# Performance work log

Measured on AMD Instinct MI355X. Metric: run time of the kernel, lower is better.

## Reference

```python
import jax, jax.numpy as jnp
import numpy as np

L = 16            # num_levels
F = 2             # features per level
T = 1 << 19       # hashmap size
BASE = 16         # base resolution
RES = 512         # desired_resolution (outer trilinear grid)
N_PTS = 262144

# 8 corner offsets of a unit cube, [8,3]
OFFS = np.array([[(c >> 0) & 1, (c >> 1) & 1, (c >> 2) & 1] for c in range(8)], dtype=np.uint32)
OFFS_J = jnp.asarray(OFFS)
OFFS_B = jnp.asarray(OFFS.astype(bool))
P1 = jnp.uint32(2654435761)
P2 = jnp.uint32(805459861)


def hash_encode(x01, table):
    """Instant-NGP multiresolution hash encoding. x01: [N,3] in [0,1]. table: [L,T,F]."""
    feats = []
    for l in range(L):
        res = BASE * (2 ** l)
        pos = x01 * res                      # [N,3]
        p0 = jnp.floor(pos)
        frac = pos - p0                      # [N,3]
        corners = p0.astype(jnp.uint32)[:, None, :] + OFFS_J[None]   # [N,8,3]
        if (res + 1) ** 3 <= T:              # dense level
            c = jnp.minimum(corners, jnp.uint32(res))
            idx = c[..., 0] + c[..., 1] * jnp.uint32(res + 1) + c[..., 2] * jnp.uint32((res + 1) * (res + 1))
        else:                                # hashed level (spatial hash, xor of primes)
            idx = corners[..., 0] ^ (corners[..., 1] * P1) ^ (corners[..., 2] * P2)
            idx = idx & jnp.uint32(T - 1)
        g = table[l][idx.astype(jnp.int32)]  # [N,8,F]
        w = jnp.where(OFFS_B[None], frac[:, None, :], 1.0 - frac[:, None, :]).prod(-1)  # [N,8]
        feats.append(jnp.einsum('nc,ncf->nf', w, g))
    return jnp.concatenate(feats, axis=-1)   # [N, L*F]


def mlp(x, W0, W1, W2):
    h = jax.nn.relu(x @ W0)
    h = jax.nn.relu(h @ W1)
    return h @ W2


def setup_inputs() -> dict:
    key = jax.random.key(0)
    k1, k2, k3, k4, k5 = jax.random.split(key, 5)
    xyz = jax.random.uniform(k1, (N_PTS, 3), dtype=jnp.float32, minval=-1.0, maxval=1.0)
    table = jax.random.uniform(k2, (L, T, F), dtype=jnp.float32, minval=-1e-4, maxval=1e-4)
    W0 = jax.random.normal(k3, (L * F, 64), dtype=jnp.float32) * (1.0 / np.sqrt(L * F))
    W1 = jax.random.normal(k4, (64, 64), dtype=jnp.float32) * (1.0 / 8.0)
    W2 = jax.random.normal(k5, (64, 8), dtype=jnp.float32) * (1.0 / 8.0)
    return {"xyz": xyz, "table": table, "W0": W0, "W1": W1, "W2": W2, "bound": 1}


def reference(xyz, table, W0, W1, W2, bound):
    xn = (xyz + bound) / (2 * bound)          # [N,3] in [0,1]
    coords = xn * RES
    c0 = jnp.clip(jnp.floor(coords), 0.0, RES - 1.0)   # [N,3] floats holding ints
    frac = coords - c0                         # u,v,w per-axis [N,3]
    out = jnp.zeros((xyz.shape[0], 8), dtype=xyz.dtype)
    for b in range(8):
        bits = np.array([(b >> 0) & 1, (b >> 1) & 1, (b >> 2) & 1], dtype=np.float32)
        cc = (c0 + bits) / RES                 # corner point normalized to [0,1]
        f = mlp(hash_encode(cc, table), W0, W1, W2)   # [N,8]
        w = jnp.where(bits.astype(bool), frac, 1.0 - frac).prod(-1)  # [N]
        out = out + w[:, None] * f
    return out
```

## Files before the change

### kernel.cpp

```cpp
#include <hip/hip_runtime.h>


typedef __attribute__((ext_vector_type(8))) short short8_t;
typedef __attribute__((ext_vector_type(4))) float f32x4;
typedef unsigned long long ull;

static constexpr unsigned kT    = 1u << 19;
static constexpr unsigned kMask = kT - 1u;
static constexpr unsigned cP1   = 2654435761u;
static constexpr unsigned cP2   = 805459861u;
static constexpr int      BLOCK = 256;
static constexpr int      TOFF  = 4096;
static constexpr unsigned CMB   = 1u << 20;
static constexpr unsigned SMF   = 1u << 21;
static constexpr unsigned D01   = (1u << 21) + (1u << 17);
static constexpr unsigned N01   = 35937u;
static constexpr unsigned D2    = D01 + 72000u;
static constexpr unsigned N2    = 274625u;
static constexpr unsigned PARTO = 2621440u;
static constexpr size_t   WS_NEED2 = ((size_t)PARTO + (1u << 22)) * 4;

static __device__ __forceinline__ unsigned bf16_rn(float x) {
    unsigned u = __float_as_uint(x);
    return (u + 0x7fffu + ((u >> 16) & 1u)) >> 16;
}

static __device__ __forceinline__ float2 bf2dec(unsigned u) {
    return make_float2(__uint_as_float(u << 16),
                       __uint_as_float(u & 0xffff0000u));
}

static __device__ __forceinline__ unsigned cvtpk(float lo, float hi) {
    unsigned r;
    asm("v_cvt_pk_bf16_f32 %0, %1, %2" : "=v"(r) : "v"(lo), "v"(hi));
    return r;
}

static __device__ __forceinline__ unsigned pkbf(ull e) {
    return bf16_rn(__uint_as_float((unsigned)e))
         | (bf16_rn(__uint_as_float((unsigned)(e >> 32))) << 16);
}

static __device__ __forceinline__ f32x4 mfma16(short8_t a, short8_t b, f32x4 c) {
    return __builtin_amdgcn_mfma_f32_16x16x32_bf16(a, b, c, 0, 0, 0);
}

__global__ __launch_bounds__(256)
void prep_all(const float* __restrict__ W0, const float* __restrict__ W1,
              const float* __restrict__ W2, const float2* __restrict__ tbl,
              unsigned* __restrict__ ws, int ncc, int ncb, int nsf, int ncd,
              int nc01)
{
    const int bx = blockIdx.x, tid = threadIdx.x;
    if (bx < ncc) {
        const int i = bx * 256 + tid;
        const ull* __restrict__ p = (const ull*)(tbl + (size_t)3 * kT);
        const ull a = __builtin_nontemporal_load(p + 2 * (size_t)i);
        const ull b = __builtin_nontemporal_load(p + 2 * (size_t)i + 1);
        ((ull*)(ws + TOFF))[i] = (ull)pkbf(a) | ((ull)pkbf(b) << 32);
    } else if (bx < ncc + ncb) {
        const unsigned j = (unsigned)((bx - ncc) * 256 + tid);
        unsigned dw[8];
        #pragma unroll
        for (int b = 0; b < 4; ++b) {
            const ull e = __builtin_nontemporal_load(
                (const ull*)tbl + (size_t)5 * kT + (j | ((unsigned)b << 17)));
            dw[b] = pkbf(e);
        }
        #pragma unroll
        for (int b = 0; b < 2; ++b) {
            const ull e = __builtin_nontemporal_load(
                (const ull*)tbl + (size_t)6 * kT
                + ((size_t)(j | ((unsigned)b << 17)) << 1));
            dw[4 + b] = pkbf(e);
        }
        {
            const ull e = __builtin_nontemporal_load(
                (const ull*)tbl + (size_t)7 * kT + ((size_t)j << 2));
            dw[6] = pkbf(e);
            dw[7] = 0u;
        }
        uint4* dst = (uint4*)(ws + TOFF + CMB + j * 8);
        dst[0] = make_uint4(dw[0], dw[1], dw[2], dw[3]);
        dst[1] = make_uint4(dw[4], dw[5], dw[6], dw[7]);
    } else if (bx < ncc + ncb + nsf) {
        const int i = (bx - ncc - ncb) * 256 + tid;
        const unsigned v = 131071u - (unsigned)i;
        const int s = __clz((int)v) - 12;
        const unsigned fo = (1u << 17) - (1u << (20 - s));
        const unsigned j = (unsigned)i - fo;
        const ull e = __builtin_nontemporal_load(
            (const ull*)tbl + ((size_t)(5 + s) << 19) + ((size_t)j << s));
        ws[TOFF + SMF + i] = pkbf(e);
    } else if (bx < ncc + ncb + nsf + ncd) {
        const int i = (bx - ncc - ncb - nsf) * 256 + tid;
        if (i < (int)N2) {
            const ull e = __builtin_nontemporal_load(
                (const ull*)tbl + (size_t)2 * kT + i);
            ws[TOFF + D2 + i] = pkbf(e);
        }
    } else if (bx < ncc + ncb + nsf + ncd + nc01) {
        const int i = (bx - ncc - ncb - nsf - ncd) * 256 + tid;
        if (i < (int)N01) {
            const int vz = i / 1089;
            const int r  = i - vz * 1089;
            const int vy = r / 33;
            const int vx = r - vy * 33;
            const float2 f1 = tbl[(size_t)kT + i];
            const int x0 = vx >> 1, y0 = vy >> 1, z0 = vz >> 1;
            const int x1 = (x0 + 1 > 16) ? 16 : x0 + 1;
            const int y1 = (y0 + 1 > 16) ? 16 : y0 + 1;
            const int z1 = (z0 + 1 > 16) ? 16 : z0 + 1;
            const float fx = (vx & 1) ? 0.5f : 0.0f;
            const float fy = (vy & 1) ? 0.5f : 0.0f;
            const float fz = (vz & 1) ? 0.5f : 0.0f;
            const int Y0 = y0 * 17, Y1 = y1 * 17, Z0 = z0 * 289, Z1 = z1 * 289;
            const float2 g0 = tbl[x0 + Y0 + Z0], g1 = tbl[x1 + Y0 + Z0];
            const float2 g2 = tbl[x0 + Y1 + Z0], g3 = tbl[x1 + Y1 + Z0];
            const float2 g4 = tbl[x0 + Y0 + Z1], g5 = tbl[x1 + Y0 + Z1];
            const float2 g6 = tbl[x0 + Y1 + Z1], g7 = tbl[x1 + Y1 + Z1];
            const float wx1 = fx, wx0 = 1.0f - fx;
            const float wy1 = fy, wy0 = 1.0f - fy;
            const float wz1 = fz, wz0 = 1.0f - fz;
            const float w00 = wx0 * wy0, w10 = wx1 * wy0, w01 = wx0 * wy1, w11 = wx1 * wy1;
            const float a0 = w00 * wz0, a1 = w10 * wz0, a2 = w01 * wz0, a3 = w11 * wz0;
            const float a4 = w00 * wz1, a5 = w10 * wz1, a6 = w01 * wz1, a7 = w11 * wz1;
            const float f0x = a0 * g0.x + a1 * g1.x + a2 * g2.x + a3 * g3.x
                            + a4 * g4.x + a5 * g5.x + a6 * g6.x + a7 * g7.x;
            const float f0y = a0 * g0.y + a1 * g1.y + a2 * g2.y + a3 * g3.y
                            + a4 * g4.y + a5 * g5.y + a6 * g6.y + a7 * g7.y;
            ((ull*)(ws + TOFF + D01))[i] =
                (ull)cvtpk(f0x, f0y) | ((ull)cvtpk(f1.x, f1.y) << 32);
        }
    } else {
        const int t = (bx - ncc - ncb - nsf - ncd - nc01) * 4 + (tid >> 6);
        if (t >= 14) return;
        const int lane = tid & 63;
        const int n = lane & 15, q = lane >> 4;
        unsigned hi[4];
        #pragma unroll
        for (int d = 0; d < 4; ++d) {
            unsigned h2[2];
            #pragma unroll
            for (int s = 0; s < 2; ++s) {
                const int j = d * 2 + s;
                float v;
                if (t < 4) {
                    v = W0[(q * 8 + j) * 64 + t * 16 + n];
                } else {
                    const int kp = (j < 4) ? (q * 4 + j) : (16 + q * 4 + (j - 4));
                    if (t < 12) v = W1[(((t - 4) & 1) * 32 + kp) * 64 + ((t - 4) >> 1) * 16 + n];
                    else        v = (n < 8) ? W2[((t - 12) * 32 + kp) * 8 + n] : 0.0f;
                }
                h2[s] = bf16_rn(v);
            }
            hi[d] = h2[0] | (h2[1] << 16);
        }
        ((uint4*)ws)[t * 64 + lane] = make_uint4(hi[0], hi[1], hi[2], hi[3]);
    }
}

__global__ __launch_bounds__(256, 8)
void ngp_pa(const float* __restrict__ xyz, const int* __restrict__ boundp,
            unsigned* __restrict__ ws)
{
    const int tid = threadIdx.x;
    const int ge  = blockIdx.x * 256 + tid;
    const int pt  = ge >> 3;
    const int b   = ge & 7;

    const float bnd = (float)boundp[0];
    const float sc  = 0.5f / bnd;
    const float pxv = __builtin_nontemporal_load(xyz + pt * 3 + 0);
    const float pyv = __builtin_nontemporal_load(xyz + pt * 3 + 1);
    const float pzv = __builtin_nontemporal_load(xyz + pt * 3 + 2);
    const float cxf = (pxv + bnd) * sc * 512.0f;
    const float cyf = (pyv + bnd) * sc * 512.0f;
    const float czf = (pzv + bnd) * sc * 512.0f;
    const float c0x = fminf(fmaxf(floorf(cxf), 0.0f), 511.0f);
    const float c0y = fminf(fmaxf(floorf(cyf), 0.0f), 511.0f);
    const float c0z = fminf(fmaxf(floorf(czf), 0.0f), 511.0f);
    const unsigned kx = (unsigned)c0x + (unsigned)(b & 1);
    const unsigned ky = (unsigned)c0y + (unsigned)((b >> 1) & 1);
    const unsigned kz = (unsigned)c0z + (unsigned)((b >> 2) & 1);

    const unsigned* __restrict__ tbx = ws + TOFF;
    unsigned gH[2][8];
    #pragma unroll
    for (int l = 3; l < 5; ++l) {
        const int d = 5 - l;
        const unsigned qx = kx >> d, qy = ky >> d, qz = kz >> d;
        const unsigned hy0 = qy * cP1, hy1 = hy0 + cP1;
        const unsigned hz0 = qz * cP2, hz1 = hz0 + cP2;
        const unsigned x1u = qx + 1u;
        unsigned hidx[8];
        hidx[0] = (qx  ^ hy0 ^ hz0) & kMask;  hidx[1] = (x1u ^ hy0 ^ hz0) & kMask;
        hidx[2] = (qx  ^ hy1 ^ hz0) & kMask;  hidx[3] = (x1u ^ hy1 ^ hz0) & kMask;
        hidx[4] = (qx  ^ hy0 ^ hz1) & kMask;  hidx[5] = (x1u ^ hy0 ^ hz1) & kMask;
        hidx[6] = (qx  ^ hy1 ^ hz1) & kMask;  hidx[7] = (x1u ^ hy1 ^ hz1) & kMask;
        const unsigned* __restrict__ base = tbx + (size_t)(l - 3) * kT;
        #pragma unroll
        for (int c = 0; c < 8; ++c) gH[l - 3][c] = base[hidx[c]];
    }

    unsigned xd34[2];
    #pragma unroll
    for (int l = 3; l < 5; ++l) {
        const int d = 5 - l;
        const unsigned m = (1u << d) - 1u;
        const float inv = 1.0f / (float)(1 << d);
        const float fx = (float)(kx & m) * inv;
        const float fy = (float)(ky & m) * inv;
        const float fz = (float)(kz & m) * inv;
        const float2 g0 = bf2dec(gH[l - 3][0]), g1 = bf2dec(gH[l - 3][1]);
        const float2 g2 = bf2dec(gH[l - 3][2]), g3 = bf2dec(gH[l - 3][3]);
        const float2 g4 = bf2dec(gH[l - 3][4]), g5 = bf2dec(gH[l - 3][5]);
        const float2 g6 = bf2dec(gH[l - 3][6]), g7 = bf2dec(gH[l - 3][7]);
        const float wx1 = fx, wx0 = 1.0f - fx;
        const float wy1 = fy, wy0 = 1.0f - fy;
        const float wz1 = fz, wz0 = 1.0f - fz;
        const float w00 = wx0 * wy0, w10 = wx1 * wy0, w01 = wx0 * wy1, w11 = wx1 * wy1;
        const float a0 = w00 * wz0, a1 = w10 * wz0, a2 = w01 * wz0, a3 = w11 * wz0;
        const float a4 = w00 * wz1, a5 = w10 * wz1, a6 = w01 * wz1, a7 = w11 * wz1;
        const float vx = a0 * g0.x + a1 * g1.x + a2 * g2.x + a3 * g3.x
                       + a4 * g4.x + a5 * g5.x + a6 * g6.x + a7 * g7.x;
        const float vy = a0 * g0.y + a1 * g1.y + a2 * g2.y + a3 * g3.y
                       + a4 * g4.y + a5 * g5.y + a6 * g6.y + a7 * g7.y;
        xd34[l - 3] = cvtpk(vx, vy);
    }
    ((ull*)(ws + PARTO))[ge] = (ull)xd34[0] | ((ull)xd34[1] << 32);
}

__global__ __launch_bounds__(BLOCK, 5)
void ngp_pb(const float*  __restrict__ xyz,
            const int*    __restrict__ boundp,
            const unsigned* __restrict__ wsw,
            float*        __restrict__ out)
{
    __shared__ __align__(16) unsigned lds[4096];
    const int tid  = threadIdx.x;
    const int lane = tid & 63;
    const int wv   = tid >> 6;
    const int col  = lane & 15;
    const int q    = lane >> 4;
    const int swz  = (tid ^ (tid >> 2) ^ (tid >> 4)) & 3;

    const unsigned* __restrict__ tbx = wsw + TOFF;
    const float bnd = (float)boundp[0];
    const float sc  = 0.5f / bnd;
    const f32x4 zero = {0.0f, 0.0f, 0.0f, 0.0f};

    const int ge = blockIdx.x * BLOCK + tid;
    const int pt = ge >> 3;
    const int b  = ge & 7;

    const float pxv = __builtin_nontemporal_load(xyz + pt * 3 + 0);
    const float pyv = __builtin_nontemporal_load(xyz + pt * 3 + 1);
    const float pzv = __builtin_nontemporal_load(xyz + pt * 3 + 2);
    const float cxf = (pxv + bnd) * sc * 512.0f;
    const float cyf = (pyv + bnd) * sc * 512.0f;
    const float czf = (pzv + bnd) * sc * 512.0f;
    const float c0x = fminf(fmaxf(floorf(cxf), 0.0f), 511.0f);
    const float c0y = fminf(fmaxf(floorf(cyf), 0.0f), 511.0f);
    const float c0z = fminf(fmaxf(floorf(czf), 0.0f), 511.0f);
    const float frx = cxf - c0x;
    const float fry = cyf - c0y;
    const float frz = czf - c0z;

    const unsigned kx = (unsigned)c0x + (unsigned)(b & 1);
    const unsigned ky = (unsigned)c0y + (unsigned)((b >> 1) & 1);
    const unsigned kz = (unsigned)c0z + (unsigned)((b >> 2) & 1);

    const float wb = ((b & 1) ? frx : 1.0f - frx)
                   * ((b & 2) ? fry : 1.0f - fry)
                   * ((b & 4) ? frz : 1.0f - frz);

    const unsigned kyp = ky * cP1;
    const unsigned kzp = kz * cP2;
    const unsigned X   = kx ^ kyp ^ kzp;

    const unsigned j17 = X & ((1u << 17) - 1u);
    const uint4 rc0 = *(const uint4*)(tbx + CMB + j17 * 8);
    const uint4 rc1 = *(const uint4*)(tbx + CMB + j17 * 8 + 4);

    unsigned gsm[8];
    #pragma unroll
    for (int l = 8; l < 16; ++l) {
        const int s = l - 5;
        const unsigned fo = (1u << 17) - (1u << (20 - s));
        gsm[l - 8] = tbx[SMF + fo + (X & ((1u << (19 - s)) - 1u))];
    }

    const ull pv = ((const ull*)(wsw + PARTO))[ge];

    unsigned xd[16];
    {
        const unsigned qx = kx >> 4, qy = ky >> 4, qz = kz >> 4;
        const float fx = (float)(kx & 15u) * 0.0625f;
        const float fy = (float)(ky & 15u) * 0.0625f;
        const float fz = (float)(kz & 15u) * 0.0625f;
        const unsigned x0 = qx, x1 = (qx + 1u > 32u) ? 32u : qx + 1u;
        const unsigned y0 = qy * 33u, y1 = ((qy + 1u > 32u) ? 32u : qy + 1u) * 33u;
        const unsigned z0 = qz * 1089u, z1 = ((qz + 1u > 32u) ? 32u : qz + 1u) * 1089u;
        const uint2* __restrict__ b01 = (const uint2*)(tbx + D01);
        const uint2 h0 = b01[x0 + y0 + z0], h1 = b01[x1 + y0 + z0];
        const uint2 h2 = b01[x0 + y1 + z0], h3 = b01[x1 + y1 + z0];
        const uint2 h4 = b01[x0 + y0 + z1], h5 = b01[x1 + y0 + z1];
        const uint2 h6 = b01[x0 + y1 + z1], h7 = b01[x1 + y1 + z1];
        const float wx1 = fx, wx0 = 1.0f - fx;
        const float wy1 = fy, wy0 = 1.0f - fy;
        const float wz1 = fz, wz0 = 1.0f - fz;
        const float w00 = wx0 * wy0, w10 = wx1 * wy0, w01 = wx0 * wy1, w11 = wx1 * wy1;
        const float a0 = w00 * wz0, a1 = w10 * wz0, a2 = w01 * wz0, a3 = w11 * wz0;
        const float a4 = w00 * wz1, a5 = w10 * wz1, a6 = w01 * wz1, a7 = w11 * wz1;
        float f0x, f0y, f1x, f1y;
        float2 d;
        d = bf2dec(h0.x); f0x  = a0 * d.x; f0y  = a0 * d.y;
        d = bf2dec(h0.y); f1x  = a0 * d.x; f1y  = a0 * d.y;
        d = bf2dec(h1.x); f0x += a1 * d.x; f0y += a1 * d.y;
        d = bf2dec(h1.y); f1x += a1 * d.x; f1y += a1 * d.y;
        d = bf2dec(h2.x); f0x += a2 * d.x; f0y += a2 * d.y;
        d = bf2dec(h2.y); f1x += a2 * d.x; f1y += a2 * d.y;
        d = bf2dec(h3.x); f0x += a3 * d.x; f0y += a3 * d.y;
        d = bf2dec(h3.y); f1x += a3 * d.x; f1y += a3 * d.y;
        d = bf2dec(h4.x); f0x += a4 * d.x; f0y += a4 * d.y;
        d = bf2dec(h4.y); f1x += a4 * d.x; f1y += a4 * d.y;
        d = bf2dec(h5.x); f0x += a5 * d.x; f0y += a5 * d.y;
        d = bf2dec(h5.y); f1x += a5 * d.x; f1y += a5 * d.y;
        d = bf2dec(h6.x); f0x += a6 * d.x; f0y += a6 * d.y;
        d = bf2dec(h6.y); f1x += a6 * d.x; f1y += a6 * d.y;
        d = bf2dec(h7.x); f0x += a7 * d.x; f0y += a7 * d.y;
        d = bf2dec(h7.y); f1x += a7 * d.x; f1y += a7 * d.y;
        xd[0] = cvtpk(f0x, f0y);
        xd[1] = cvtpk(f1x, f1y);
    }
    {
        const unsigned qx = kx >> 3, qy = ky >> 3, qz = kz >> 3;
        const float fx = (float)(kx & 7u) * 0.125f;
        const float fy = (float)(ky & 7u) * 0.125f;
        const float fz = (float)(kz & 7u) * 0.125f;
        const unsigned x0 = qx, x1 = (qx + 1u > 64u) ? 64u : qx + 1u;
        const unsigned y0 = qy * 65u, y1 = ((qy + 1u > 64u) ? 64u : qy + 1u) * 65u;
        const unsigned z0 = qz * 4225u, z1 = ((qz + 1u > 64u) ? 64u : qz + 1u) * 4225u;
        const unsigned* __restrict__ b2 = tbx + D2;
        const float2 g0 = bf2dec(b2[x0 + y0 + z0]), g1 = bf2dec(b2[x1 + y0 + z0]);
        const float2 g2 = bf2dec(b2[x0 + y1 + z0]), g3 = bf2dec(b2[x1 + y1 + z0]);
        const float2 g4 = bf2dec(b2[x0 + y0 + z1]), g5 = bf2dec(b2[x1 + y0 + z1]);
        const float2 g6 = bf2dec(b2[x0 + y1 + z1]), g7 = bf2dec(b2[x1 + y1 + z1]);
        const float wx1 = fx, wx0 = 1.0f - fx;
        const float wy1 = fy, wy0 = 1.0f - fy;
        const float wz1 = fz, wz0 = 1.0f - fz;
        const float w00 = wx0 * wy0, w10 = wx1 * wy0, w01 = wx0 * wy1, w11 = wx1 * wy1;
        const float a0 = w00 * wz0, a1 = w10 * wz0, a2 = w01 * wz0, a3 = w11 * wz0;
        const float a4 = w00 * wz1, a5 = w10 * wz1, a6 = w01 * wz1, a7 = w11 * wz1;
        const float vx = a0 * g0.x + a1 * g1.x + a2 * g2.x + a3 * g3.x
                       + a4 * g4.x + a5 * g5.x + a6 * g6.x + a7 * g7.x;
        const float vy = a0 * g0.y + a1 * g1.y + a2 * g2.y + a3 * g3.y
                       + a4 * g4.y + a5 * g5.y + a6 * g6.y + a7 * g7.y;
        xd[2] = cvtpk(vx, vy);
    }
    xd[3] = (unsigned)pv;
    xd[4] = (unsigned)(pv >> 32);
    {
        const unsigned b56 = (X >> 17) & 3u;
        xd[5] = (b56 & 2u) ? ((b56 & 1u) ? rc0.w : rc0.z)
                           : ((b56 & 1u) ? rc0.y : rc0.x);
        xd[6] = ((X >> 17) & 1u) ? rc1.y : rc1.x;
        xd[7] = rc1.z;
    }
    #pragma unroll
    for (int l = 8; l < 16; ++l) xd[l] = gsm[l - 8];

    {
        uint4* xrow = (uint4*)(lds + tid * 16);
        xrow[swz]     = make_uint4(xd[0],  xd[1],  xd[2],  xd[3]);
        xrow[swz ^ 1] = make_uint4(xd[4],  xd[5],  xd[6],  xd[7]);
        xrow[swz ^ 2] = make_uint4(xd[8],  xd[9],  xd[10], xd[11]);
        xrow[swz ^ 3] = make_uint4(xd[12], xd[13], xd[14], xd[15]);
    }

    asm volatile("s_waitcnt lgkmcnt(0)" ::: "memory");
    __builtin_amdgcn_sched_barrier(0);

    short8_t w[14];
    {
        const short8_t* __restrict__ wfr = (const short8_t*)wsw;
        #pragma unroll
        for (int t = 0; t < 14; ++t) w[t] = wfr[t * 64 + lane];
    }

    #pragma unroll 1
    for (int g = 0; g < 4; ++g) {
        const int ev  = wv * 64 + g * 16 + col;
        const int esw = ((ev ^ (ev >> 2) ^ (ev >> 4)) & 3) ^ q;
        const short8_t xb = *(const short8_t*)(lds + ev * 16 + esw * 4);
        const float wbv = __shfl(wb, g * 16 + col, 64);

        unsigned hp0[4], hp1[4];
        #pragma unroll
        for (int mt = 0; mt < 4; ++mt) {
            f32x4 a = mfma16(w[mt], xb, zero);
            hp0[mt] = cvtpk(fmaxf(a[0], 0.0f), fmaxf(a[1], 0.0f));
            hp1[mt] = cvtpk(fmaxf(a[2], 0.0f), fmaxf(a[3], 0.0f));
        }
        uint4 u0 = make_uint4(hp0[0], hp1[0], hp0[1], hp1[1]);
        uint4 u1 = make_uint4(hp0[2], hp1[2], hp0[3], hp1[3]);
        short8_t bk0 = *(short8_t*)&u0;
        short8_t bk1 = *(short8_t*)&u1;

        #pragma unroll
        for (int mt = 0; mt < 4; ++mt) {
            f32x4 a = mfma16(w[4 + mt * 2], bk0, zero);
            a = mfma16(w[5 + mt * 2], bk1, a);
            hp0[mt] = cvtpk(fmaxf(a[0], 0.0f), fmaxf(a[1], 0.0f));
            hp1[mt] = cvtpk(fmaxf(a[2], 0.0f), fmaxf(a[3], 0.0f));
        }
        u0 = make_uint4(hp0[0], hp1[0], hp0[1], hp1[1]);
        u1 = make_uint4(hp0[2], hp1[2], hp0[3], hp1[3]);
        bk0 = *(short8_t*)&u0;
        bk1 = *(short8_t*)&u1;

        f32x4 a3 = mfma16(w[12], bk0, zero);
        a3 = mfma16(w[13], bk1, a3);

        float v0 = wbv * a3[0], v1 = wbv * a3[1], v2 = wbv * a3[2], v3 = wbv * a3[3];
        #pragma unroll
        for (int s = 1; s < 8; s <<= 1) {
            v0 += __shfl_xor(v0, s);
            v1 += __shfl_xor(v1, s);
            v2 += __shfl_xor(v2, s);
            v3 += __shfl_xor(v3, s);
        }
        if (((lane & 7) == 0) && q < 2) {
            const int p = (blockIdx.x * BLOCK + ev) >> 3;
            ull* op = (ull*)(out + p * 8 + q * 4);
            __builtin_nontemporal_store(
                (ull)__float_as_uint(v0) | ((ull)__float_as_uint(v1) << 32), op);
            __builtin_nontemporal_store(
                (ull)__float_as_uint(v2) | ((ull)__float_as_uint(v3) << 32), op + 1);
        }
    }
}

__global__ __launch_bounds__(BLOCK, 5)
void ngp_mfma(const float*  __restrict__ xyz,
              const float2* __restrict__ tbl,
              const int*    __restrict__ boundp,
              const unsigned* __restrict__ wsw,
              float*        __restrict__ out,
              int ntiles)
{
    __shared__ __align__(16) unsigned lds[4096];
    const int tid  = threadIdx.x;
    const int lane = tid & 63;
    const int wv   = tid >> 6;
    const int col  = lane & 15;
    const int q    = lane >> 4;
    const int swz  = (tid ^ (tid >> 2) ^ (tid >> 4)) & 3;

    const float bnd = (float)boundp[0];
    const float sc  = 0.5f / bnd;
    const f32x4 zero = {0.0f, 0.0f, 0.0f, 0.0f};

    const int ge = blockIdx.x * BLOCK + tid;
    const int pt = ge >> 3;
    const int b  = ge & 7;

    const float cxf = (xyz[pt * 3 + 0] + bnd) * sc * 512.0f;
    const float cyf = (xyz[pt * 3 + 1] + bnd) * sc * 512.0f;
    const float czf = (xyz[pt * 3 + 2] + bnd) * sc * 512.0f;
    const float c0x = fminf(fmaxf(floorf(cxf), 0.0f), 511.0f);
    const float c0y = fminf(fmaxf(floorf(cyf), 0.0f), 511.0f);
    const float c0z = fminf(fmaxf(floorf(czf), 0.0f), 511.0f);
    const float frx = cxf - c0x;
    const float fry = cyf - c0y;
    const float frz = czf - c0z;

    const unsigned kx = (unsigned)c0x + (unsigned)(b & 1);
    const unsigned ky = (unsigned)c0y + (unsigned)((b >> 1) & 1);
    const unsigned kz = (unsigned)c0z + (unsigned)((b >> 2) & 1);

    const float wb = ((b & 1) ? frx : 1.0f - frx)
                   * ((b & 2) ? fry : 1.0f - fry)
                   * ((b & 4) ? frz : 1.0f - frz);

    const unsigned kyp = ky * cP1;
    const unsigned kzp = kz * cP2;
    unsigned gfu_dummy;
    (void)gfu_dummy;
    float2 gff[11];
    #pragma unroll
    for (int l = 5; l < 16; ++l) {
        const int s = l - 5;
        const unsigned idx = ((kx << s) ^ (kyp << s) ^ (kzp << s)) & kMask;
        gff[l - 5] = tbl[(size_t)l * kT + idx];
    }

    float2 gHf[2][8];
    #pragma unroll
    for (int l = 3; l < 5; ++l) {
        const int d = 5 - l;
        const unsigned qx = kx >> d, qy = ky >> d, qz = kz >> d;
        const unsigned hy0 = qy * cP1, hy1 = hy0 + cP1;
        const unsigned hz0 = qz * cP2, hz1 = hz0 + cP2;
        const unsigned x1u = qx + 1u;
        unsigned hidx[8];
        hidx[0] = (qx  ^ hy0 ^ hz0) & kMask;  hidx[1] = (x1u ^ hy0 ^ hz0) & kMask;
        hidx[2] = (qx  ^ hy1 ^ hz0) & kMask;  hidx[3] = (x1u ^ hy1 ^ hz0) & kMask;
        hidx[4] = (qx  ^ hy0 ^ hz1) & kMask;  hidx[5] = (x1u ^ hy0 ^ hz1) & kMask;
        hidx[6] = (qx  ^ hy1 ^ hz1) & kMask;  hidx[7] = (x1u ^ hy1 ^ hz1) & kMask;
        const float2* __restrict__ base = tbl + (size_t)l * kT;
        #pragma unroll
        for (int c = 0; c < 8; ++c) gHf[l - 3][c] = base[hidx[c]];
    }

    float2 gc[5];
    #pragma unroll
    for (int l = 0; l < 5; ++l) {
        const int d = 5 - l;
        const unsigned m = (1u << d) - 1u;
        const float inv = 1.0f / (float)(1 << d);
        const unsigned qx = kx >> d, qy = ky >> d, qz = kz >> d;
        const float fx = (float)(kx & m) * inv;
        const float fy = (float)(ky & m) * inv;
        const float fz = (float)(kz & m) * inv;
        float2 g0, g1, g2, g3, g4, g5, g6, g7;
        if (l < 3) {
            const unsigned res = 16u << l;
            const unsigned R = res + 1u, R2 = R * R;
            const unsigned x0 = (qx < res ? qx : res);
            const unsigned x1 = (qx + 1u < res ? qx + 1u : res);
            const unsigned y0 = (qy < res ? qy : res) * R;
            const unsigned y1 = (qy + 1u < res ? qy + 1u : res) * R;
            const unsigned z0 = (qz < res ? qz : res) * R2;
            const unsigned z1 = (qz + 1u < res ? qz + 1u : res) * R2;
            const float2* __restrict__ base = tbl + (size_t)l * kT;
            g0 = base[x0 + y0 + z0]; g1 = base[x1 + y0 + z0];
            g2 = base[x0 + y1 + z0]; g3 = base[x1 + y1 + z0];
            g4 = base[x0 + y0 + z1]; g5 = base[x1 + y0 + z1];
            g6 = base[x0 + y1 + z1]; g7 = base[x1 + y1 + z1];
        } else {
            g0 = gHf[l - 3][0]; g1 = gHf[l - 3][1]; g2 = gHf[l - 3][2]; g3 = gHf[l - 3][3];
            g4 = gHf[l - 3][4]; g5 = gHf[l - 3][5]; g6 = gHf[l - 3][6]; g7 = gHf[l - 3][7];
        }
        const float wx1 = fx, wx0 = 1.0f - fx;
        const float wy1 = fy, wy0 = 1.0f - fy;
        const float wz1 = fz, wz0 = 1.0f - fz;
        const float w00 = wx0 * wy0, w10 = wx1 * wy0, w01 = wx0 * wy1, w11 = wx1 * wy1;
        const float a0 = w00 * wz0, a1 = w10 * wz0, a2 = w01 * wz0, a3 = w11 * wz0;
        const float a4 = w00 * wz1, a5 = w10 * wz1, a6 = w01 * wz1, a7 = w11 * wz1;
        float vx = a0 * g0.x + a1 * g1.x + a2 * g2.x + a3 * g3.x
                 + a4 * g4.x + a5 * g5.x + a6 * g6.x + a7 * g7.x;
        float vy = a0 * g0.y + a1 * g1.y + a2 * g2.y + a3 * g3.y
                 + a4 * g4.y + a5 * g5.y + a6 * g6.y + a7 * g7.y;
        gc[l] = make_float2(vx, vy);
    }

    unsigned xd[16];
    #pragma unroll
    for (int l = 0; l < 5; ++l)
        xd[l] = cvtpk(gc[l].x, gc[l].y);
    #pragma unroll
    for (int l = 5; l < 16; ++l)
        xd[l] = cvtpk(gff[l - 5].x, gff[l - 5].y);
    {
        uint4* xrow = (uint4*)(lds + tid * 16);
        xrow[swz]     = make_uint4(xd[0],  xd[1],  xd[2],  xd[3]);
        xrow[swz ^ 1] = make_uint4(xd[4],  xd[5],  xd[6],  xd[7]);
        xrow[swz ^ 2] = make_uint4(xd[8],  xd[9],  xd[10], xd[11]);
        xrow[swz ^ 3] = make_uint4(xd[12], xd[13], xd[14], xd[15]);
    }

    asm volatile("s_waitcnt lgkmcnt(0)" ::: "memory");
    __builtin_amdgcn_sched_barrier(0);

    short8_t w[14];
    {
        const short8_t* __restrict__ wfr = (const short8_t*)wsw;
        #pragma unroll
        for (int t = 0; t < 14; ++t) w[t] = wfr[t * 64 + lane];
    }

    #pragma unroll 1
    for (int g = 0; g < 4; ++g) {
        const int ev  = wv * 64 + g * 16 + col;
        const int esw = ((ev ^ (ev >> 2) ^ (ev >> 4)) & 3) ^ q;
        const short8_t xb = *(const short8_t*)(lds + ev * 16 + esw * 4);
        const float wbv = __shfl(wb, g * 16 + col, 64);

        unsigned hp0[4], hp1[4];
        #pragma unroll
        for (int mt = 0; mt < 4; ++mt) {
            f32x4 a = mfma16(w[mt], xb, zero);
            hp0[mt] = cvtpk(fmaxf(a[0], 0.0f), fmaxf(a[1], 0.0f));
            hp1[mt] = cvtpk(fmaxf(a[2], 0.0f), fmaxf(a[3], 0.0f));
        }
        uint4 u0 = make_uint4(hp0[0], hp1[0], hp0[1], hp1[1]);
        uint4 u1 = make_uint4(hp0[2], hp1[2], hp0[3], hp1[3]);
        short8_t bk0 = *(short8_t*)&u0;
        short8_t bk1 = *(short8_t*)&u1;

        #pragma unroll
        for (int mt = 0; mt < 4; ++mt) {
            f32x4 a = mfma16(w[4 + mt * 2], bk0, zero);
            a = mfma16(w[5 + mt * 2], bk1, a);
            hp0[mt] = cvtpk(fmaxf(a[0], 0.0f), fmaxf(a[1], 0.0f));
            hp1[mt] = cvtpk(fmaxf(a[2], 0.0f), fmaxf(a[3], 0.0f));
        }
        u0 = make_uint4(hp0[0], hp1[0], hp0[1], hp1[1]);
        u1 = make_uint4(hp0[2], hp1[2], hp0[3], hp1[3]);
        bk0 = *(short8_t*)&u0;
        bk1 = *(short8_t*)&u1;

        f32x4 a3 = mfma16(w[12], bk0, zero);
        a3 = mfma16(w[13], bk1, a3);

        float v0 = wbv * a3[0], v1 = wbv * a3[1], v2 = wbv * a3[2], v3 = wbv * a3[3];
        #pragma unroll
        for (int s = 1; s < 8; s <<= 1) {
            v0 += __shfl_xor(v0, s);
            v1 += __shfl_xor(v1, s);
            v2 += __shfl_xor(v2, s);
            v3 += __shfl_xor(v3, s);
        }
        if (((lane & 7) == 0) && q < 2) {
            const int p = (blockIdx.x * BLOCK + ev) >> 3;
            *(float4*)(out + p * 8 + q * 4) = make_float4(v0, v1, v2, v3);
        }
    }
}

extern "C" void kernel_launch(void* const* d_in, const int* in_sizes, int n_in,
                              void* d_out, int out_size, void* d_ws, size_t ws_size,
                              hipStream_t stream) {
    const float*  xyz = (const float*)d_in[0];
    const float2* tbl = (const float2*)d_in[1];
    const float*  W0  = (const float*)d_in[2];
    const float*  W1  = (const float*)d_in[3];
    const float*  W2  = (const float*)d_in[4];
    const int*    bnd = (const int*)d_in[5];
    float* out = (float*)d_out;

    const int npts   = in_sizes[0] / 3;
    const int total  = npts * 8;
    const int ntiles = total / BLOCK;

    const bool big2 = (ws_size >= WS_NEED2);
    const int ncc  = big2 ? (1 << 19) / 256 : 0;
    const int ncb  = big2 ? (1 << 17) / 256 : 0;
    const int nsf  = big2 ? 130560 / 256 : 0;
    const int ncd  = big2 ? (int)((N2 + 255u) / 256u) : 0;
    const int nc01 = big2 ? (int)((N01 + 255u) / 256u) : 0;

    hipLaunchKernelGGL(prep_all, dim3(ncc + ncb + nsf + ncd + nc01 + 4),
                       dim3(256), 0, stream, W0, W1, W2, tbl, (unsigned*)d_ws,
                       ncc, ncb, nsf, ncd, nc01);

    if (big2) {
        hipLaunchKernelGGL(ngp_pa, dim3(total / 256), dim3(256), 0, stream,
                           xyz, bnd, (unsigned*)d_ws);
        hipLaunchKernelGGL(ngp_pb, dim3(ntiles), dim3(BLOCK), 0, stream,
                           xyz, bnd, (const unsigned*)d_ws, out);
    } else {
        hipLaunchKernelGGL(ngp_mfma, dim3(ntiles), dim3(BLOCK), 0, stream,
                           xyz, tbl, bnd, (const unsigned*)d_ws, out, ntiles);
    }
}
```

Measured before the change: 215.8 us.

## Group hashed levels 8-15 into packed slabs and pair x-neighbors in dense tables

The prep kernel now packs the small hashed levels 8-15 into grouped 32-byte or 16-byte records indexed by the shared hash bits, so the main kernel issues a few vector loads instead of eight scattered scalar loads. The dense level 0/1 and level 2 tables are also rebuilt so each entry stores its x+1 neighbor, which halves the number of gathers per trilinear lookup. The costs are a larger workspace footprint, extra prep work, and duplicated data in the precomputed tables.

```diff
diff --git a/kernel.cpp b/kernel.cpp
--- a/kernel.cpp
+++ b/kernel.cpp
@@ -12,12 +12,14 @@
 static constexpr int      BLOCK = 256;
 static constexpr int      TOFF  = 4096;
 static constexpr unsigned CMB   = 1u << 20;
-static constexpr unsigned SMF   = 1u << 21;
-static constexpr unsigned D01   = (1u << 21) + (1u << 17);
+static constexpr unsigned GB    = 1u << 21;
+static constexpr unsigned GC    = GB + (1u << 17);
+static constexpr unsigned GD    = GC + (1u << 14);
+static constexpr unsigned P01   = GD + (1u << 11);
 static constexpr unsigned N01   = 35937u;
-static constexpr unsigned D2    = D01 + 72000u;
+static constexpr unsigned P2    = P01 + N01 * 4u;
 static constexpr unsigned N2    = 274625u;
-static constexpr unsigned PARTO = 2621440u;
+static constexpr unsigned PARTO = 2949120u;
 static constexpr size_t   WS_NEED2 = ((size_t)PARTO + (1u << 22)) * 4;
 
 static __device__ __forceinline__ unsigned bf16_rn(float x) {
@@ -41,99 +43,145 @@
          | (bf16_rn(__uint_as_float((unsigned)(e >> 32))) << 16);
 }
 
+static __device__ __forceinline__ unsigned sel4(uint4 v, unsigned b) {
+    const unsigned lo = (b & 1u) ? v.y : v.x;
+    const unsigned hi = (b & 1u) ? v.w : v.z;
+    return (b & 2u) ? hi : lo;
+}
+
 static __device__ __forceinline__ f32x4 mfma16(short8_t a, short8_t b, f32x4 c) {
     return __builtin_amdgcn_mfma_f32_16x16x32_bf16(a, b, c, 0, 0, 0);
+}
+
+static __device__ uint2 f01_vert(const float2* __restrict__ tbl,
+                                 int vx, int vy, int vz)
+{
+    const float2 f1 = tbl[(size_t)kT + vz * 1089 + vy * 33 + vx];
+    const int x0 = vx >> 1, y0 = vy >> 1, z0 = vz >> 1;
+    const int x1 = (x0 + 1 > 16) ? 16 : x0 + 1;
+    const int y1 = (y0 + 1 > 16) ? 16 : y0 + 1;
+    const int z1 = (z0 + 1 > 16) ? 16 : z0 + 1;
+    const float fx = (vx & 1) ? 0.5f : 0.0f;
+    const float fy = (vy & 1) ? 0.5f : 0.0f;
+    const float fz = (vz & 1) ? 0.5f : 0.0f;
+    const int Y0 = y0 * 17, Y1 = y1 * 17, Z0 = z0 * 289, Z1 = z1 * 289;
+    const float2 g0 = tbl[x0 + Y0 + Z0], g1 = tbl[x1 + Y0 + Z0];
+    const float2 g2 = tbl[x0 + Y1 + Z0], g3 = tbl[x1 + Y1 + Z0];
+    const float2 g4 = tbl[x0 + Y0 + Z1], g5 = tbl[x1 + Y0 + Z1];
+    const float2 g6 = tbl[x0 + Y1 + Z1], g7 = tbl[x1 + Y1 + Z1];
+    const float wx1 = fx, wx0 = 1.0f - fx;
+    const float wy1 = fy, wy0 = 1.0f - fy;
+    const float wz1 = fz, wz0 = 1.0f - fz;
+    const float w00 = wx0 * wy0, w10 = wx1 * wy0, w01 = wx0 * wy1, w11 = wx1 * wy1;
+    const float a0 = w00 * wz0, a1 = w10 * wz0, a2 = w01 * wz0, a3 = w11 * wz0;
+    const float a4 = w00 * wz1, a5 = w10 * wz1, a6 = w01 * wz1, a7 = w11 * wz1;
+    const float f0x = a0 * g0.x + a1 * g1.x + a2 * g2.x + a3 * g3.x
+                    + a4 * g4.x + a5 * g5.x + a6 * g6.x + a7 * g7.x;
+    const float f0y = a0 * g0.y + a1 * g1.y + a2 * g2.y + a3 * g3.y
+                    + a4 * g4.y + a5 * g5.y + a6 * g6.y + a7 * g7.y;
+    return make_uint2(cvtpk(f0x, f0y), cvtpk(f1.x, f1.y));
 }
 
 __global__ __launch_bounds__(256)
 void prep_all(const float* __restrict__ W0, const float* __restrict__ W1,
               const float* __restrict__ W2, const float2* __restrict__ tbl,
-              unsigned* __restrict__ ws, int ncc, int ncb, int nsf, int ncd,
-              int nc01)
+              unsigned* __restrict__ ws,
+              int ncc, int ncA, int ncB, int ncC, int ncD, int nP01, int nP2)
 {
     const int bx = blockIdx.x, tid = threadIdx.x;
+    const ull* __restrict__ t8 = (const ull*)tbl;
     if (bx < ncc) {
         const int i = bx * 256 + tid;
-        const ull* __restrict__ p = (const ull*)(tbl + (size_t)3 * kT);
+        const ull* __restrict__ p = t8 + (size_t)3 * kT;
         const ull a = __builtin_nontemporal_load(p + 2 * (size_t)i);
         const ull b = __builtin_nontemporal_load(p + 2 * (size_t)i + 1);
         ((ull*)(ws + TOFF))[i] = (ull)pkbf(a) | ((ull)pkbf(b) << 32);
-    } else if (bx < ncc + ncb) {
+    } else if (bx < ncc + ncA) {
         const unsigned j = (unsigned)((bx - ncc) * 256 + tid);
         unsigned dw[8];
         #pragma unroll
-        for (int b = 0; b < 4; ++b) {
-            const ull e = __builtin_nontemporal_load(
-                (const ull*)tbl + (size_t)5 * kT + (j | ((unsigned)b << 17)));
-            dw[b] = pkbf(e);
-        }
-        #pragma unroll
-        for (int b = 0; b < 2; ++b) {
-            const ull e = __builtin_nontemporal_load(
-                (const ull*)tbl + (size_t)6 * kT
-                + ((size_t)(j | ((unsigned)b << 17)) << 1));
-            dw[4 + b] = pkbf(e);
-        }
-        {
-            const ull e = __builtin_nontemporal_load(
-                (const ull*)tbl + (size_t)7 * kT + ((size_t)j << 2));
-            dw[6] = pkbf(e);
-            dw[7] = 0u;
-        }
+        for (int b = 0; b < 4; ++b)
+            dw[b] = pkbf(__builtin_nontemporal_load(
+                t8 + (size_t)5 * kT + (j | ((unsigned)b << 17))));
+        #pragma unroll
+        for (int b = 0; b < 2; ++b)
+            dw[4 + b] = pkbf(__builtin_nontemporal_load(
+                t8 + (size_t)6 * kT + ((size_t)(j | ((unsigned)b << 17)) << 1)));
+        dw[6] = pkbf(__builtin_nontemporal_load(
+                t8 + (size_t)7 * kT + ((size_t)j << 2)));
+        dw[7] = 0u;
         uint4* dst = (uint4*)(ws + TOFF + CMB + j * 8);
         dst[0] = make_uint4(dw[0], dw[1], dw[2], dw[3]);
         dst[1] = make_uint4(dw[4], dw[5], dw[6], dw[7]);
-    } else if (bx < ncc + ncb + nsf) {
-        const int i = (bx - ncc - ncb) * 256 + tid;
-        const unsigned v = 131071u - (unsigned)i;
-        const int s = __clz((int)v) - 12;
-        const unsigned fo = (1u << 17) - (1u << (20 - s));
-        const unsigned j = (unsigned)i - fo;
-        const ull e = __builtin_nontemporal_load(
-            (const ull*)tbl + ((size_t)(5 + s) << 19) + ((size_t)j << s));
-        ws[TOFF + SMF + i] = pkbf(e);
-    } else if (bx < ncc + ncb + nsf + ncd) {
-        const int i = (bx - ncc - ncb - nsf) * 256 + tid;
-        if (i < (int)N2) {
-            const ull e = __builtin_nontemporal_load(
-                (const ull*)tbl + (size_t)2 * kT + i);
-            ws[TOFF + D2 + i] = pkbf(e);
-        }
-    } else if (bx < ncc + ncb + nsf + ncd + nc01) {
-        const int i = (bx - ncc - ncb - nsf - ncd) * 256 + tid;
+    } else if (bx < ncc + ncA + ncB) {
+        const unsigned j = (unsigned)((bx - ncc - ncA) * 256 + tid);
+        unsigned dw[8];
+        #pragma unroll
+        for (int b = 0; b < 4; ++b)
+            dw[b] = pkbf(__builtin_nontemporal_load(
+                t8 + (size_t)8 * kT + ((size_t)(j | ((unsigned)b << 14)) << 3)));
+        #pragma unroll
+        for (int b = 0; b < 2; ++b)
+            dw[4 + b] = pkbf(__builtin_nontemporal_load(
+                t8 + (size_t)9 * kT + ((size_t)(j | ((unsigned)b << 14)) << 4)));
+        dw[6] = pkbf(__builtin_nontemporal_load(
+                t8 + (size_t)10 * kT + ((size_t)j << 5)));
+        dw[7] = 0u;
+        uint4* dst = (uint4*)(ws + TOFF + GB + j * 8);
+        dst[0] = make_uint4(dw[0], dw[1], dw[2], dw[3]);
+        dst[1] = make_uint4(dw[4], dw[5], dw[6], dw[7]);
+    } else if (bx < ncc + ncA + ncB + ncC) {
+        const unsigned j = (unsigned)((bx - ncc - ncA - ncB) * 256 + tid);
+        unsigned dw[8];
+        #pragma unroll
+        for (int b = 0; b < 4; ++b)
+            dw[b] = pkbf(__builtin_nontemporal_load(
+                t8 + (size_t)11 * kT + ((size_t)(j | ((unsigned)b << 11)) << 6)));
+        #pragma unroll
+        for (int b = 0; b < 2; ++b)
+            dw[4 + b] = pkbf(__builtin_nontemporal_load(
+                t8 + (size_t)12 * kT + ((size_t)(j | ((unsigned)b << 11)) << 7)));
+        dw[6] = pkbf(__builtin_nontemporal_load(
+                t8 + (size_t)13 * kT + ((size_t)j << 8)));
+        dw[7] = 0u;
+        uint4* dst = (uint4*)(ws + TOFF + GC + j * 8);
+        dst[0] = make_uint4(dw[0], dw[1], dw[2], dw[3]);
+        dst[1] = make_uint4(dw[4], dw[5], dw[6], dw[7]);
+    } else if (bx < ncc + ncA + ncB + ncC + ncD) {
+        const unsigned j = (unsigned)((bx - ncc - ncA - ncB - ncC) * 256 + tid);
+        unsigned dw[4];
+        #pragma unroll
+        for (int b = 0; b < 2; ++b)
+            dw[b] = pkbf(__builtin_nontemporal_load(
+                t8 + (size_t)14 * kT + ((size_t)(j | ((unsigned)b << 9)) << 9)));
+        dw[2] = pkbf(__builtin_nontemporal_load(
+                t8 + (size_t)15 * kT + ((size_t)j << 10)));
+        dw[3] = 0u;
+        ((uint4*)(ws + TOFF + GD))[j] = make_uint4(dw[0], dw[1], dw[2], dw[3]);
+    } else if (bx < ncc + ncA + ncB + ncC + ncD + nP01) {
+        const int i = (bx - ncc - ncA - ncB - ncC - ncD) * 256 + tid;
         if (i < (int)N01) {
             const int vz = i / 1089;
             const int r  = i - vz * 1089;
             const int vy = r / 33;
             const int vx = r - vy * 33;
-            const float2 f1 = tbl[(size_t)kT + i];
-            const int x0 = vx >> 1, y0 = vy >> 1, z0 = vz >> 1;
-            const int x1 = (x0 + 1 > 16) ? 16 : x0 + 1;
-            const int y1 = (y0 + 1 > 16) ? 16 : y0 + 1;
-            const int z1 = (z0 + 1 > 16) ? 16 : z0 + 1;
-            const float fx = (vx & 1) ? 0.5f : 0.0f;
-            const float fy = (vy & 1) ? 0.5f : 0.0f;
-            const float fz = (vz & 1) ? 0.5f : 0.0f;
-            const int Y0 = y0 * 17, Y1 = y1 * 17, Z0 = z0 * 289, Z1 = z1 * 289;
-            const float2 g0 = tbl[x0 + Y0 + Z0], g1 = tbl[x1 + Y0 + Z0];
-            const float2 g2 = tbl[x0 + Y1 + Z0], g3 = tbl[x1 + Y1 + Z0];
-            const float2 g4 = tbl[x0 + Y0 + Z1], g5 = tbl[x1 + Y0 + Z1];
-            const float2 g6 = tbl[x0 + Y1 + Z1], g7 = tbl[x1 + Y1 + Z1];
-            const float wx1 = fx, wx0 = 1.0f - fx;
-            const float wy1 = fy, wy0 = 1.0f - fy;
-            const float wz1 = fz, wz0 = 1.0f - fz;
-            const float w00 = wx0 * wy0, w10 = wx1 * wy0, w01 = wx0 * wy1, w11 = wx1 * wy1;
-            const float a0 = w00 * wz0, a1 = w10 * wz0, a2 = w01 * wz0, a3 = w11 * wz0;
-            const float a4 = w00 * wz1, a5 = w10 * wz1, a6 = w01 * wz1, a7 = w11 * wz1;
-            const float f0x = a0 * g0.x + a1 * g1.x + a2 * g2.x + a3 * g3.x
-                            + a4 * g4.x + a5 * g5.x + a6 * g6.x + a7 * g7.x;
-            const float f0y = a0 * g0.y + a1 * g1.y + a2 * g2.y + a3 * g3.y
-                            + a4 * g4.y + a5 * g5.y + a6 * g6.y + a7 * g7.y;
-            ((ull*)(ws + TOFF + D01))[i] =
-                (ull)cvtpk(f0x, f0y) | ((ull)cvtpk(f1.x, f1.y) << 32);
+            const uint2 a = f01_vert(tbl, vx, vy, vz);
+            const uint2 b = f01_vert(tbl, (vx + 1 > 32) ? 32 : vx + 1, vy, vz);
+            ((uint4*)(ws + TOFF + P01))[i] = make_uint4(a.x, a.y, b.x, b.y);
+        }
+    } else if (bx < ncc + ncA + ncB + ncC + ncD + nP01 + nP2) {
+        const int i = (bx - ncc - ncA - ncB - ncC - ncD - nP01) * 256 + tid;
+        if (i < (int)N2) {
+            const int x = i % 65;
+            const unsigned lo = pkbf(__builtin_nontemporal_load(
+                t8 + (size_t)2 * kT + i));
+            const unsigned hi = pkbf(__builtin_nontemporal_load(
+                t8 + (size_t)2 * kT + i + (x < 64 ? 1 : 0)));
+            ((ull*)(ws + TOFF + P2))[i] = (ull)lo | ((ull)hi << 32);
         }
     } else {
-        const int t = (bx - ncc - ncb - nsf - ncd - nc01) * 4 + (tid >> 6);
+        const int t = (bx - ncc - ncA - ncB - ncC - ncD - nP01 - nP2) * 4
+                    + (tid >> 6);
         if (t >= 14) return;
         const int lane = tid & 63;
         const int n = lane & 15, q = lane >> 4;
@@ -280,16 +328,16 @@
     const unsigned X   = kx ^ kyp ^ kzp;
 
     const unsigned j17 = X & ((1u << 17) - 1u);
-    const uint4 rc0 = *(const uint4*)(tbx + CMB + j17 * 8);
-    const uint4 rc1 = *(const uint4*)(tbx + CMB + j17 * 8 + 4);
-
-    unsigned gsm[8];
-    #pragma unroll
-    for (int l = 8; l < 16; ++l) {
-        const int s = l - 5;
-        const unsigned fo = (1u << 17) - (1u << (20 - s));
-        gsm[l - 8] = tbx[SMF + fo + (X & ((1u << (19 - s)) - 1u))];
-    }
+    const uint4 rA0 = *(const uint4*)(tbx + CMB + j17 * 8);
+    const uint4 rA1 = *(const uint4*)(tbx + CMB + j17 * 8 + 4);
+    const unsigned j14 = X & ((1u << 14) - 1u);
+    const uint4 rB0 = *(const uint4*)(tbx + GB + j14 * 8);
+    const uint4 rB1 = *(const uint4*)(tbx + GB + j14 * 8 + 4);
+    const unsigned j11 = X & ((1u << 11) - 1u);
+    const uint4 rC0 = *(const uint4*)(tbx + GC + j11 * 8);
+    const uint4 rC1 = *(const uint4*)(tbx + GC + j11 * 8 + 4);
+    const unsigned j9 = X & ((1u << 9) - 1u);
+    const uint4 rD = ((const uint4*)(tbx + GD))[j9];
 
     const ull pv = ((const ull*)(wsw + PARTO))[ge];
 
@@ -299,38 +347,26 @@
         const float fx = (float)(kx & 15u) * 0.0625f;
         const float fy = (float)(ky & 15u) * 0.0625f;
         const float fz = (float)(kz & 15u) * 0.0625f;
-        const unsigned x0 = qx, x1 = (qx + 1u > 32u) ? 32u : qx + 1u;
+        const unsigned x0 = qx;
         const unsigned y0 = qy * 33u, y1 = ((qy + 1u > 32u) ? 32u : qy + 1u) * 33u;
         const unsigned z0 = qz * 1089u, z1 = ((qz + 1u > 32u) ? 32u : qz + 1u) * 1089u;
-        const uint2* __restrict__ b01 = (const uint2*)(tbx + D01);
-        const uint2 h0 = b01[x0 + y0 + z0], h1 = b01[x1 + y0 + z0];
-        const uint2 h2 = b01[x0 + y1 + z0], h3 = b01[x1 + y1 + z0];
-        const uint2 h4 = b01[x0 + y0 + z1], h5 = b01[x1 + y0 + z1];
-        const uint2 h6 = b01[x0 + y1 + z1], h7 = b01[x1 + y1 + z1];
+        const uint4* __restrict__ p01 = (const uint4*)(tbx + P01);
+        const uint4 h00 = p01[x0 + y0 + z0], h10 = p01[x0 + y1 + z0];
+        const uint4 h01 = p01[x0 + y0 + z1], h11 = p01[x0 + y1 + z1];
         const float wx1 = fx, wx0 = 1.0f - fx;
         const float wy1 = fy, wy0 = 1.0f - fy;
         const float wz1 = fz, wz0 = 1.0f - fz;
-        const float w00 = wx0 * wy0, w10 = wx1 * wy0, w01 = wx0 * wy1, w11 = wx1 * wy1;
-        const float a0 = w00 * wz0, a1 = w10 * wz0, a2 = w01 * wz0, a3 = w11 * wz0;
-        const float a4 = w00 * wz1, a5 = w10 * wz1, a6 = w01 * wz1, a7 = w11 * wz1;
-        float f0x, f0y, f1x, f1y;
-        float2 d;
-        d = bf2dec(h0.x); f0x  = a0 * d.x; f0y  = a0 * d.y;
-        d = bf2dec(h0.y); f1x  = a0 * d.x; f1y  = a0 * d.y;
-        d = bf2dec(h1.x); f0x += a1 * d.x; f0y += a1 * d.y;
-        d = bf2dec(h1.y); f1x += a1 * d.x; f1y += a1 * d.y;
-        d = bf2dec(h2.x); f0x += a2 * d.x; f0y += a2 * d.y;
-        d = bf2dec(h2.y); f1x += a2 * d.x; f1y += a2 * d.y;
-        d = bf2dec(h3.x); f0x += a3 * d.x; f0y += a3 * d.y;
-        d = bf2dec(h3.y); f1x += a3 * d.x; f1y += a3 * d.y;
-        d = bf2dec(h4.x); f0x += a4 * d.x; f0y += a4 * d.y;
-        d = bf2dec(h4.y); f1x += a4 * d.x; f1y += a4 * d.y;
-        d = bf2dec(h5.x); f0x += a5 * d.x; f0y += a5 * d.y;
-        d = bf2dec(h5.y); f1x += a5 * d.x; f1y += a5 * d.y;
-        d = bf2dec(h6.x); f0x += a6 * d.x; f0y += a6 * d.y;
-        d = bf2dec(h6.y); f1x += a6 * d.x; f1y += a6 * d.y;
-        d = bf2dec(h7.x); f0x += a7 * d.x; f0y += a7 * d.y;
-        d = bf2dec(h7.y); f1x += a7 * d.x; f1y += a7 * d.y;
+        float f0x = 0.0f, f0y = 0.0f, f1x = 0.0f, f1y = 0.0f;
+        #define ACC01(h, wyz) { \
+            const float wl = (wyz) * wx0, wh = (wyz) * wx1; \
+            float2 d; \
+            d = bf2dec((h).x); f0x += wl * d.x; f0y += wl * d.y; \
+            d = bf2dec((h).z); f0x += wh * d.x; f0y += wh * d.y; \
+            d = bf2dec((h).y); f1x += wl * d.x; f1y += wl * d.y; \
+            d = bf2dec((h).w); f1x += wh * d.x; f1y += wh * d.y; }
+        ACC01(h00, wy0 * wz0); ACC01(h10, wy1 * wz0);
+        ACC01(h01, wy0 * wz1); ACC01(h11, wy1 * wz1);
+        #undef ACC01
         xd[0] = cvtpk(f0x, f0y);
         xd[1] = cvtpk(f1x, f1y);
     }
@@ -339,37 +375,39 @@
         const float fx = (float)(kx & 7u) * 0.125f;
         const float fy = (float)(ky & 7u) * 0.125f;
         const float fz = (float)(kz & 7u) * 0.125f;
-        const unsigned x0 = qx, x1 = (qx + 1u > 64u) ? 64u : qx + 1u;
+        const unsigned x0 = qx;
         const unsigned y0 = qy * 65u, y1 = ((qy + 1u > 64u) ? 64u : qy + 1u) * 65u;
         const unsigned z0 = qz * 4225u, z1 = ((qz + 1u > 64u) ? 64u : qz + 1u) * 4225u;
-        const unsigned* __restrict__ b2 = tbx + D2;
-        const float2 g0 = bf2dec(b2[x0 + y0 + z0]), g1 = bf2dec(b2[x1 + y0 + z0]);
-        const float2 g2 = bf2dec(b2[x0 + y1 + z0]), g3 = bf2dec(b2[x1 + y1 + z0]);
-        const float2 g4 = bf2dec(b2[x0 + y0 + z1]), g5 = bf2dec(b2[x1 + y0 + z1]);
-        const float2 g6 = bf2dec(b2[x0 + y1 + z1]), g7 = bf2dec(b2[x1 + y1 + z1]);
+        const ull* __restrict__ p2 = (const ull*)(tbx + P2);
+        const ull e00 = p2[x0 + y0 + z0], e10 = p2[x0 + y1 + z0];
+        const ull e01 = p2[x0 + y0 + z1], e11 = p2[x0 + y1 + z1];
         const float wx1 = fx, wx0 = 1.0f - fx;
         const float wy1 = fy, wy0 = 1.0f - fy;
         const float wz1 = fz, wz0 = 1.0f - fz;
-        const float w00 = wx0 * wy0, w10 = wx1 * wy0, w01 = wx0 * wy1, w11 = wx1 * wy1;
-        const float a0 = w00 * wz0, a1 = w10 * wz0, a2 = w01 * wz0, a3 = w11 * wz0;
-        const float a4 = w00 * wz1, a5 = w10 * wz1, a6 = w01 * wz1, a7 = w11 * wz1;
-        const float vx = a0 * g0.x + a1 * g1.x + a2 * g2.x + a3 * g3.x
-                       + a4 * g4.x + a5 * g5.x + a6 * g6.x + a7 * g7.x;
-        const float vy = a0 * g0.y + a1 * g1.y + a2 * g2.y + a3 * g3.y
-                       + a4 * g4.y + a5 * g5.y + a6 * g6.y + a7 * g7.y;
-        xd[2] = cvtpk(vx, vy);
+        float vx_ = 0.0f, vy_ = 0.0f;
+        #define ACC2(e, wyz) { \
+            const float wl = (wyz) * wx0, wh = (wyz) * wx1; \
+            const float2 dl = bf2dec((unsigned)(e)); \
+            const float2 dh = bf2dec((unsigned)((e) >> 32)); \
+            vx_ += wl * dl.x + wh * dh.x; vy_ += wl * dl.y + wh * dh.y; }
+        ACC2(e00, wy0 * wz0); ACC2(e10, wy1 * wz0);
+        ACC2(e01, wy0 * wz1); ACC2(e11, wy1 * wz1);
+        #undef ACC2
+        xd[2] = cvtpk(vx_, vy_);
     }
     xd[3] = (unsigned)pv;
     xd[4] = (unsigned)(pv >> 32);
-    {
-        const unsigned b56 = (X >> 17) & 3u;
-        xd[5] = (b56 & 2u) ? ((b56 & 1u) ? rc0.w : rc0.z)
-                           : ((b56 & 1u) ? rc0.y : rc0.x);
-        xd[6] = ((X >> 17) & 1u) ? rc1.y : rc1.x;
-        xd[7] = rc1.z;
-    }
-    #pragma unroll
-    for (int l = 8; l < 16; ++l) xd[l] = gsm[l - 8];
+    xd[5]  = sel4(rA0, (X >> 17) & 3u);
+    xd[6]  = ((X >> 17) & 1u) ? rA1.y : rA1.x;
+    xd[7]  = rA1.z;
+    xd[8]  = sel4(rB0, (X >> 14) & 3u);
+    xd[9]  = ((X >> 14) & 1u) ? rB1.y : rB1.x;
+    xd[10] = rB1.z;
+    xd[11] = sel4(rC0, (X >> 11) & 3u);
+    xd[12] = ((X >> 11) & 1u) ? rC1.y : rC1.x;
+    xd[13] = rC1.z;
+    xd[14] = ((X >> 9) & 1u) ? rD.y : rD.x;
+    xd[15] = rD.z;
 
     {
         uint4* xrow = (uint4*)(lds + tid * 16);
@@ -486,8 +524,6 @@
 
     const unsigned kyp = ky * cP1;
     const unsigned kzp = kz * cP2;
-    unsigned gfu_dummy;
-    (void)gfu_dummy;
     float2 gff[11];
     #pragma unroll
     for (int l = 5; l < 16; ++l) {
@@ -647,14 +683,17 @@
 
     const bool big2 = (ws_size >= WS_NEED2);
     const int ncc  = big2 ? (1 << 19) / 256 : 0;
-    const int ncb  = big2 ? (1 << 17) / 256 : 0;
-    const int nsf  = big2 ? 130560 / 256 : 0;
-    const int ncd  = big2 ? (int)((N2 + 255u) / 256u) : 0;
-    const int nc01 = big2 ? (int)((N01 + 255u) / 256u) : 0;
-
-    hipLaunchKernelGGL(prep_all, dim3(ncc + ncb + nsf + ncd + nc01 + 4),
+    const int ncA  = big2 ? (1 << 17) / 256 : 0;
+    const int ncB  = big2 ? (1 << 14) / 256 : 0;
+    const int ncC  = big2 ? (1 << 11) / 256 : 0;
+    const int ncD  = big2 ? 2 : 0;
+    const int nP01 = big2 ? (int)((N01 + 255u) / 256u) : 0;
+    const int nP2  = big2 ? (int)((N2 + 255u) / 256u) : 0;
+
+    hipLaunchKernelGGL(prep_all,
+                       dim3(ncc + ncA + ncB + ncC + ncD + nP01 + nP2 + 4),
                        dim3(256), 0, stream, W0, W1, W2, tbl, (unsigned*)d_ws,
-                       ncc, ncb, nsf, ncd, nc01);
+                       ncc, ncA, ncB, ncC, ncD, nP01, nP2);
 
     if (big2) {
         hipLaunchKernelGGL(ngp_pa, dim3(total / 256), dim3(256), 0, stream,
```

Result: faster. 198.8 us (-7.9%).
